# Kernel tuning notes

Measured on AMD Instinct MI355X. Metric: run time of the kernel, lower is better.

Reference implementation:

```python
import jax, jax.numpy as jnp
import numpy as np
from jax import lax

CHAOS_R = 3.5699456
N_STEPS = 10


def setup_inputs() -> dict:
    key = jax.random.key(0)
    k1, k2, k3 = jax.random.split(key, 3)
    B, T, D = 256, 8192, 5
    x = jax.random.normal(k1, (B, T, D), dtype=jnp.float32)
    temple = jax.random.normal(k2, (4, 5), dtype=jnp.float32)
    breath_vector = jax.random.normal(k3, (5,), dtype=jnp.float32)
    return {"x": x, "temple": temple, "breath_vector": breath_vector}


def reference(x, temple, breath_vector):
    # x: (B, T, D) with D == 5
    B, T, D = x.shape

    # mirror_sequence: chaos logistic map on mean of x[0,0]
    seed = jnp.mod(jnp.mean(x[0, 0]), 1.0)
    chaos = CHAOS_R * seed * (1.0 - seed)
    mirrored = jnp.where(chaos > 0.7, 9.0 - x,
                         jnp.where(chaos > 0.4, jnp.flip(x, axis=1), x))
    mode_code = jnp.where(chaos > 0.7, 0, jnp.where(chaos > 0.4, 1, 2))  # 0=invert,1=retrograde,2=none

    extended_x = jnp.concatenate([x, mirrored], axis=1)  # (B, 2T, D)

    # per-token breath: first T tokens use breath[:4], mirrored half uses breath[1:5]
    breath_main = breath_vector[:4]
    breath_mirror = breath_vector[1:5]
    breath = jnp.concatenate([
        jnp.broadcast_to(breath_main, (T, 4)),
        jnp.broadcast_to(breath_mirror, (T, 4)),
    ], axis=0)  # (2T, 4)

    def step(vec, _):
        # vec: (B, 2T, 5)
        transformed = jnp.einsum('rd,btd->btr', temple, vec)  # (B, 2T, 4)
        resonance = jnp.sum(transformed * breath[None, :, :], axis=-1)  # (B, 2T)
        vec = jnp.roll(vec, shift=1, axis=-1).at[..., 0].set(jnp.mod(resonance, 10.0))
        return vec, resonance

    vec0 = extended_x[..., :5]
    _, history = lax.scan(step, vec0, None, length=N_STEPS)  # (10, B, 2T)

    # torch.std default is unbiased (ddof=1)
    score = 1.0 / (1.0 + jnp.std(history, axis=0, ddof=1))  # (B, 2T)
    gate_weights = score[..., None]  # (B, 2T, 1)
    return gate_weights, extended_x, mode_code
```

## Files before the change

### kernel.cpp

```cpp
#include <hip/hip_runtime.h>

constexpr int B_DIM = 256, T_DIM = 8192;
constexpr long long GATE_N = (long long)B_DIM * 2 * T_DIM;
constexpr long long EXT_N  = GATE_N * 5;

__global__ void temple_setup(const float* __restrict__ x, const float* __restrict__ temple,
                             const float* __restrict__ breath,
                             float* __restrict__ out, double* __restrict__ w) {
    if (threadIdx.x != 0) return;
    double s = 0.0;
    for (int d = 0; d < 5; ++d) s += (double)x[d];
    s = s / 5.0;
    double seed  = s - floor(s);
    double chaos = 3.5699456 * seed * (1.0 - seed);
    int mode = (chaos > 0.7) ? 0 : ((chaos > 0.4) ? 1 : 2);
    for (int d = 0; d < 5; ++d) {
        double a = 0.0, c = 0.0;
        for (int r = 0; r < 4; ++r) {
            double tv = (double)temple[r * 5 + d];
            a += (double)breath[r]     * tv;
            c += (double)breath[r + 1] * tv;
        }
        w[d] = a; w[5 + d] = c;
    }
    w[10] = (double)mode;
    out[GATE_N + EXT_N] = (float)mode;
}

__global__ __launch_bounds__(256) void temple_main(const float* __restrict__ x,
                                                   const double* __restrict__ w,
                                                   float* __restrict__ out) {
    const int k  = threadIdx.x;
    const int b  = blockIdx.x >> 5;
    const int t0 = (blockIdx.x & 31) << 8;
    const int mode = (int)w[10];
    const long long rowBase = (long long)b * (2 * T_DIM);
    float* gate = out;
    float* ext  = out + GATE_N;

    const float4* __restrict__ src4 = (const float4*)(x + ((long long)b * T_DIM + t0) * 5);
    const bool extra = (k < 64);
    float4 c0 = src4[k];
    float4 c1;
    if (extra) c1 = src4[256 + k];

    float4* dmain = (float4*)(ext + (rowBase + t0) * 5);
    dmain[k] = c0;
    if (extra) dmain[256 + k] = c1;
    if (mode == 0) {
        float4* dmir = (float4*)(ext + (rowBase + T_DIM + t0) * 5);
        dmir[k] = make_float4(9.f - c0.x, 9.f - c0.y, 9.f - c0.z, 9.f - c0.w);
        if (extra) dmir[256 + k] = make_float4(9.f - c1.x, 9.f - c1.y, 9.f - c1.z, 9.f - c1.w);
    } else if (mode == 2) {
        float4* dmir = (float4*)(ext + (rowBase + T_DIM + t0) * 5);
        dmir[k] = c0;
        if (extra) dmir[256 + k] = c1;
    }

    const int t = t0 + k;
    const float* __restrict__ xi = x + ((long long)b * T_DIM + t) * 5;
    const float x0 = xi[0], x1 = xi[1], x2 = xi[2], x3 = xi[3], x4 = xi[4];

    if (mode == 1) {
        float* dm = ext + (rowBase + 2 * T_DIM - 1 - t) * 5;
        dm[0] = x0; dm[1] = x1; dm[2] = x2; dm[3] = x3; dm[4] = x4;
    }

    const double wa0 = w[0], wa1 = w[1], wa2 = w[2], wa3 = w[3], wa4 = w[4];
    const double wb0 = w[5], wb1 = w[6], wb2 = w[7], wb3 = w[8], wb4 = w[9];
    double a0 = x0, a1 = x1, a2 = x2, a3 = x3, a4 = x4;
    double b0, b1, b2, b3, b4;
    if (mode == 0) { b0 = 9.0 - a0; b1 = 9.0 - a1; b2 = 9.0 - a2; b3 = 9.0 - a3; b4 = 9.0 - a4; }
    else           { b0 = a0; b1 = a1; b2 = a2; b3 = a3; b4 = a4; }

    float ha[10], hb[10];
#pragma unroll
    for (int s = 0; s < 10; ++s) {
        double ra = a0 * wa0;
        ra = fma(a1, wa1, ra); ra = fma(a2, wa2, ra); ra = fma(a3, wa3, ra); ra = fma(a4, wa4, ra);
        double rb = b0 * wb0;
        rb = fma(b1, wb1, rb); rb = fma(b2, wb2, rb); rb = fma(b3, wb3, rb); rb = fma(b4, wb4, rb);
        ha[s] = (float)ra; hb[s] = (float)rb;
        double qa = floor(ra * 0.1), ma = fma(qa, -10.0, ra);
        ma = (ma < 0.0) ? ma + 10.0 : ma;  ma = (ma >= 10.0) ? ma - 10.0 : ma;
        double qb = floor(rb * 0.1), mb = fma(qb, -10.0, rb);
        mb = (mb < 0.0) ? mb + 10.0 : mb;  mb = (mb >= 10.0) ? mb - 10.0 : mb;
        a4 = a3; a3 = a2; a2 = a1; a1 = a0; a0 = ma;
        b4 = b3; b3 = b2; b2 = b1; b1 = b0; b0 = mb;
    }
    float meanA = 0.f, meanB = 0.f;
#pragma unroll
    for (int s = 0; s < 10; ++s) { meanA += ha[s]; meanB += hb[s]; }
    meanA *= 0.1f; meanB *= 0.1f;
    float ssdA = 0.f, ssdB = 0.f;
#pragma unroll
    for (int s = 0; s < 10; ++s) {
        float da = ha[s] - meanA; ssdA = fmaf(da, da, ssdA);
        float db = hb[s] - meanB; ssdB = fmaf(db, db, ssdB);
    }
    const float gm = 1.0f / (1.0f + sqrtf(ssdA * (1.0f / 9.0f)));
    const float gx = 1.0f / (1.0f + sqrtf(ssdB * (1.0f / 9.0f)));

    gate[rowBase + t] = gm;
    if (mode == 1) gate[rowBase + 2 * T_DIM - 1 - t] = gx;
    else           gate[rowBase + T_DIM + t] = gx;
}

extern "C" void kernel_launch(void* const* d_in, const int* in_sizes, int n_in,
                              void* d_out, int out_size, void* d_ws, size_t ws_size,
                              hipStream_t stream) {
    const float* x      = (const float*)d_in[0];
    const float* temple = (const float*)d_in[1];
    const float* breath = (const float*)d_in[2];
    float* out = (float*)d_out;
    double* w  = (double*)d_ws;

    temple_setup<<<1, 64, 0, stream>>>(x, temple, breath, out, w);
    const int blocks = (B_DIM * T_DIM) / 256;
    temple_main<<<blocks, 256, 0, stream>>>(x, w, out);
}
```

Baseline: 141.8 us.

## Fuse setup into main kernel and use nontemporal stores for outputs

Removes the single-thread setup launch: each block's thread 0 recomputes the mode and the folded temple·breath weights into shared memory, and a block barrier follows. The main-half copy is issued before the barrier to overlap it with the setup work. All output writes become nontemporal stores to reduce cache pollution from the large streaming output. This trades one kernel launch and its serialization for redundant per-block scalar setup work plus a __syncthreads.

```diff
diff --git a/kernel.cpp b/kernel.cpp
--- a/kernel.cpp
+++ b/kernel.cpp
@@ -4,66 +4,75 @@
 constexpr long long GATE_N = (long long)B_DIM * 2 * T_DIM;
 constexpr long long EXT_N  = GATE_N * 5;
 
-__global__ void temple_setup(const float* __restrict__ x, const float* __restrict__ temple,
-                             const float* __restrict__ breath,
-                             float* __restrict__ out, double* __restrict__ w) {
-    if (threadIdx.x != 0) return;
-    double s = 0.0;
-    for (int d = 0; d < 5; ++d) s += (double)x[d];
-    s = s / 5.0;
-    double seed  = s - floor(s);
-    double chaos = 3.5699456 * seed * (1.0 - seed);
-    int mode = (chaos > 0.7) ? 0 : ((chaos > 0.4) ? 1 : 2);
-    for (int d = 0; d < 5; ++d) {
-        double a = 0.0, c = 0.0;
-        for (int r = 0; r < 4; ++r) {
-            double tv = (double)temple[r * 5 + d];
-            a += (double)breath[r]     * tv;
-            c += (double)breath[r + 1] * tv;
-        }
-        w[d] = a; w[5 + d] = c;
-    }
-    w[10] = (double)mode;
-    out[GATE_N + EXT_N] = (float)mode;
-}
+typedef float f4 __attribute__((ext_vector_type(4)));
 
-__global__ __launch_bounds__(256) void temple_main(const float* __restrict__ x,
-                                                   const double* __restrict__ w,
-                                                   float* __restrict__ out) {
+__global__ __launch_bounds__(256) void temple_fused(const float* __restrict__ x,
+                                                    const float* __restrict__ temple,
+                                                    const float* __restrict__ breath,
+                                                    float* __restrict__ out) {
+    __shared__ double w[11];
     const int k  = threadIdx.x;
     const int b  = blockIdx.x >> 5;
     const int t0 = (blockIdx.x & 31) << 8;
-    const int mode = (int)w[10];
     const long long rowBase = (long long)b * (2 * T_DIM);
     float* gate = out;
     float* ext  = out + GATE_N;
 
-    const float4* __restrict__ src4 = (const float4*)(x + ((long long)b * T_DIM + t0) * 5);
+    const f4* __restrict__ src4 = (const f4*)(x + ((long long)b * T_DIM + t0) * 5);
     const bool extra = (k < 64);
-    float4 c0 = src4[k];
-    float4 c1;
+    f4 c0 = src4[k];
+    f4 c1 = {};
     if (extra) c1 = src4[256 + k];
-
-    float4* dmain = (float4*)(ext + (rowBase + t0) * 5);
-    dmain[k] = c0;
-    if (extra) dmain[256 + k] = c1;
-    if (mode == 0) {
-        float4* dmir = (float4*)(ext + (rowBase + T_DIM + t0) * 5);
-        dmir[k] = make_float4(9.f - c0.x, 9.f - c0.y, 9.f - c0.z, 9.f - c0.w);
-        if (extra) dmir[256 + k] = make_float4(9.f - c1.x, 9.f - c1.y, 9.f - c1.z, 9.f - c1.w);
-    } else if (mode == 2) {
-        float4* dmir = (float4*)(ext + (rowBase + T_DIM + t0) * 5);
-        dmir[k] = c0;
-        if (extra) dmir[256 + k] = c1;
-    }
 
     const int t = t0 + k;
     const float* __restrict__ xi = x + ((long long)b * T_DIM + t) * 5;
     const float x0 = xi[0], x1 = xi[1], x2 = xi[2], x3 = xi[3], x4 = xi[4];
 
-    if (mode == 1) {
+    f4* dmain = (f4*)(ext + (rowBase + t0) * 5);
+    __builtin_nontemporal_store(c0, dmain + k);
+    if (extra) __builtin_nontemporal_store(c1, dmain + 256 + k);
+
+    if (k == 0) {
+        double s = 0.0;
+        for (int d = 0; d < 5; ++d) s += (double)x[d];
+        s = s / 5.0;
+        double seed  = s - floor(s);
+        double chaos = 3.5699456 * seed * (1.0 - seed);
+        int mode = (chaos > 0.7) ? 0 : ((chaos > 0.4) ? 1 : 2);
+        for (int d = 0; d < 5; ++d) {
+            double a = 0.0, c = 0.0;
+            for (int r = 0; r < 4; ++r) {
+                double tv = (double)temple[r * 5 + d];
+                a += (double)breath[r]     * tv;
+                c += (double)breath[r + 1] * tv;
+            }
+            w[d] = a; w[5 + d] = c;
+        }
+        w[10] = (double)mode;
+        if (blockIdx.x == 0) out[GATE_N + EXT_N] = (float)mode;
+    }
+    __syncthreads();
+    const int mode = (int)w[10];
+
+    if (mode == 0) {
+        f4* dmir = (f4*)(ext + (rowBase + T_DIM + t0) * 5);
+        f4 m0; m0.x = 9.f - c0.x; m0.y = 9.f - c0.y; m0.z = 9.f - c0.z; m0.w = 9.f - c0.w;
+        __builtin_nontemporal_store(m0, dmir + k);
+        if (extra) {
+            f4 m1; m1.x = 9.f - c1.x; m1.y = 9.f - c1.y; m1.z = 9.f - c1.z; m1.w = 9.f - c1.w;
+            __builtin_nontemporal_store(m1, dmir + 256 + k);
+        }
+    } else if (mode == 2) {
+        f4* dmir = (f4*)(ext + (rowBase + T_DIM + t0) * 5);
+        __builtin_nontemporal_store(c0, dmir + k);
+        if (extra) __builtin_nontemporal_store(c1, dmir + 256 + k);
+    } else {
         float* dm = ext + (rowBase + 2 * T_DIM - 1 - t) * 5;
-        dm[0] = x0; dm[1] = x1; dm[2] = x2; dm[3] = x3; dm[4] = x4;
+        __builtin_nontemporal_store(x0, dm + 0);
+        __builtin_nontemporal_store(x1, dm + 1);
+        __builtin_nontemporal_store(x2, dm + 2);
+        __builtin_nontemporal_store(x3, dm + 3);
+        __builtin_nontemporal_store(x4, dm + 4);
     }
 
     const double wa0 = w[0], wa1 = w[1], wa2 = w[2], wa3 = w[3], wa4 = w[4];
@@ -101,9 +110,9 @@
     const float gm = 1.0f / (1.0f + sqrtf(ssdA * (1.0f / 9.0f)));
     const float gx = 1.0f / (1.0f + sqrtf(ssdB * (1.0f / 9.0f)));
 
-    gate[rowBase + t] = gm;
-    if (mode == 1) gate[rowBase + 2 * T_DIM - 1 - t] = gx;
-    else           gate[rowBase + T_DIM + t] = gx;
+    __builtin_nontemporal_store(gm, &gate[rowBase + t]);
+    if (mode == 1) __builtin_nontemporal_store(gx, &gate[rowBase + 2 * T_DIM - 1 - t]);
+    else           __builtin_nontemporal_store(gx, &gate[rowBase + T_DIM + t]);
 }
 
 extern "C" void kernel_launch(void* const* d_in, const int* in_sizes, int n_in,
@@ -113,9 +122,7 @@
     const float* temple = (const float*)d_in[1];
     const float* breath = (const float*)d_in[2];
     float* out = (float*)d_out;
-    double* w  = (double*)d_ws;
 
-    temple_setup<<<1, 64, 0, stream>>>(x, temple, breath, out, w);
     const int blocks = (B_DIM * T_DIM) / 256;
-    temple_main<<<blocks, 256, 0, stream>>>(x, w, out);
+    temple_fused<<<blocks, 256, 0, stream>>>(x, temple, breath, out);
 }
```

Result: no change. 141.4 us (-0.2%).
